# Optimization experiments

Measured on AMD Instinct MI355X. Metric: run time of the kernel, lower is better.

## Reference

```python
import jax, jax.numpy as jnp
import numpy as np

B, S, D, H = 1, 4096, 1024, 16
DH = D // H  # 64
SCALE = D ** 0.5  # original divides by input_dim**0.5, not head_dim**0.5


def setup_inputs() -> dict:
    key = jax.random.key(0)
    ks = jax.random.split(key, 11)
    s = lambda i, shape, sc=1.0: jax.random.normal(ks[i], shape, dtype=jnp.float32) * sc
    w_init = 1.0 / np.sqrt(D)
    return {
        "q": s(0, (B, S, D)),
        "k": s(1, (B, S, D)),
        "v": s(2, (B, S, D)),
        "Wq": s(3, (H, D, DH), w_init),
        "bq": jnp.zeros((H, DH), jnp.float32),
        "Wk": s(4, (H, D, DH), w_init),
        "bk": jnp.zeros((H, DH), jnp.float32),
        "Wv": s(5, (H, D, DH), w_init),
        "bv": jnp.zeros((H, DH), jnp.float32),
        "Wo": s(6, (D, D), w_init),
        "bo": jnp.zeros((D,), jnp.float32),
    }


def reference(q, k, v, Wq, bq, Wk, bk, Wv, bv, Wo, bo):
    # Per-head Dense projections, batched over heads: [B,S,D] x [H,D,dh] -> [B,H,S,dh]
    Q = jnp.einsum("bsd,hde->bhse", q, Wq) + bq[None, :, None, :]
    K = jnp.einsum("bsd,hde->bhse", k, Wk) + bk[None, :, None, :]
    V = jnp.einsum("bsd,hde->bhse", v, Wv) + bv[None, :, None, :]
    # Scaled dot-product attention; note scale = sqrt(input_dim) as in source
    scores = jnp.einsum("bhse,bhte->bhst", Q, K) / SCALE  # [B,H,S,S]
    attn = jax.nn.softmax(scores, axis=-1)
    out = jnp.einsum("bhst,bhte->bhse", attn, V)  # [B,H,S,dh]
    # Concat heads along feature dim (head order matches the Python loop)
    concat = out.transpose(0, 2, 1, 3).reshape(q.shape[0], q.shape[1], H * DH)
    return concat @ Wo + bo
```

## Files before the change

kernel.cpp:

```cpp
#include <hip/hip_runtime.h>
#include <hip/hip_bf16.h>

#define S_LEN 4096
#define D_MODEL 1024
#define NH 16
#define DHEAD 64
#define QSCALE 0.0450843293f

typedef __attribute__((ext_vector_type(8))) short short8;
typedef __attribute__((ext_vector_type(4))) float floatx4;

__device__ __forceinline__ unsigned short f2bf(float f) {
    unsigned int x = __float_as_uint(f);
    x += 0x7fffu + ((x >> 16) & 1u);
    return (unsigned short)(x >> 16);
}

__device__ __forceinline__ float exp2_fast(float x) {
    return __builtin_amdgcn_exp2f(x);
}

__device__ __forceinline__ void async_copy16(const unsigned short* g, unsigned short* l) {
    __builtin_amdgcn_global_load_lds(
        (const __attribute__((address_space(1))) void*)g,
        (__attribute__((address_space(3))) void*)l, 16, 0, 0);
}

__global__ __launch_bounds__(256) void prep_all(
    const float* __restrict__ q, const float* __restrict__ k,
    const float* __restrict__ v,
    const float* __restrict__ Wq, const float* __restrict__ Wk,
    const float* __restrict__ Wv, const float* __restrict__ Wo,
    unsigned short* __restrict__ dst, unsigned short* __restrict__ ws)
{
    __shared__ float L[64][65];
    const int tid = threadIdx.x;

    if (blockIdx.x < 6144) {
        long i = (long)(blockIdx.x * 256 + tid) * 8;
        int which = (int)(i >> 22);
        long off = i & ((1 << 22) - 1);
        const float* src = (which == 0) ? q : (which == 1) ? k : v;
        float4 f0 = *(const float4*)&src[off];
        float4 f1 = *(const float4*)&src[off + 4];
        uint4 o;
        o.x = (unsigned int)f2bf(f0.x) | ((unsigned int)f2bf(f0.y) << 16);
        o.y = (unsigned int)f2bf(f0.z) | ((unsigned int)f2bf(f0.w) << 16);
        o.z = (unsigned int)f2bf(f1.x) | ((unsigned int)f2bf(f1.y) << 16);
        o.w = (unsigned int)f2bf(f1.z) | ((unsigned int)f2bf(f1.w) << 16);
        *(uint4*)&dst[i] = o;
        return;
    }

    const int bx  = blockIdx.x - 6144;
    const int mat = bx >> 8;

    if (mat < 3) {
        const float* W = (mat == 0) ? Wq : (mat == 1) ? Wk : Wv;
        unsigned short* WT = ws + (size_t)mat * (1u << 20);
        int h  = (bx >> 4) & 15;
        int dt = bx & 15;
        #pragma unroll
        for (int i = 0; i < 16; i++) {
            int idx = i * 256 + tid;
            int dp = idx >> 6, e = idx & 63;
            L[e][dp] = W[h * 65536 + (dt * 64 + dp) * 64 + e];
        }
        __syncthreads();
        #pragma unroll
        for (int i = 0; i < 16; i++) {
            int idx = i * 256 + tid;
            int e = idx >> 6, dp = idx & 63;
            WT[(h * 64 + e) * 1024 + dt * 64 + dp] = f2bf(L[e][dp]);
        }
    } else {
        unsigned short* WoT = ws + (size_t)3 * (1u << 20);
        int rt = (bx >> 4) & 15;
        int ct = bx & 15;
        #pragma unroll
        for (int i = 0; i < 16; i++) {
            int idx = i * 256 + tid;
            int dp = idx >> 6, np = idx & 63;
            L[np][dp] = Wo[(rt * 64 + dp) * 1024 + ct * 64 + np];
        }
        __syncthreads();
        #pragma unroll
        for (int i = 0; i < 16; i++) {
            int idx = i * 256 + tid;
            int np = idx >> 6, dp = idx & 63;
            WoT[(ct * 64 + np) * 1024 + rt * 64 + dp] = f2bf(L[np][dp]);
        }
    }
}

#define GEMM_CORE(XPTR, WPTR)                                                   \
    for (int k0 = 0; k0 < D_MODEL; k0 += 64) {                                  \
        __syncthreads();                                                        \
        _Pragma("unroll")                                                       \
        for (int i = 0; i < 4; i++) {                                           \
            async_copy16(&XPTR[(size_t)(m0 + srow + i * 8) * D_MODEL + k0 + scol], \
                         &As[(wave * 32 + i * 8) * 64]);                        \
            async_copy16(&WPTR[(size_t)(n0 + srow + i * 8) * D_MODEL + k0 + scol], \
                         &Bs[(wave * 32 + i * 8) * 64]);                        \
        }                                                                       \
        __syncthreads();                                                        \
        _Pragma("unroll")                                                       \
        for (int ks = 0; ks < 2; ks++) {                                        \
            short8 af[4], bf[4];                                                \
            _Pragma("unroll")                                                   \
            for (int i = 0; i < 4; i++)                                         \
                af[i] = *(const short8*)&As[(wr * 64 + i * 16 + m) * 64 + ks * 32 + quad * 8]; \
            _Pragma("unroll")                                                   \
            for (int j = 0; j < 4; j++)                                         \
                bf[j] = *(const short8*)&Bs[(wc * 64 + j * 16 + m) * 64 + ks * 32 + quad * 8]; \
            _Pragma("unroll")                                                   \
            for (int i = 0; i < 4; i++) {                                       \
                _Pragma("unroll")                                               \
                for (int j = 0; j < 4; j++)                                     \
                    acc[i][j] = __builtin_amdgcn_mfma_f32_16x16x32_bf16(af[i], bf[j], acc[i][j], 0, 0, 0); \
            }                                                                   \
        }                                                                       \
    }

__global__ __launch_bounds__(256) void qkv_gemm(
    const unsigned short* __restrict__ Xbase, const unsigned short* __restrict__ WTbase,
    const float* __restrict__ bq, const float* __restrict__ bk,
    const float* __restrict__ bv,
    unsigned short* __restrict__ Qbuf, unsigned short* __restrict__ Kbuf,
    unsigned short* __restrict__ Vbuf)
{
    __shared__ __align__(16) unsigned short As[128 * 64];
    __shared__ __align__(16) unsigned short Bs[128 * 64];

    const int z = blockIdx.z;
    const unsigned short* X  = Xbase + (size_t)z * (4u << 20);
    const unsigned short* WT = WTbase + (size_t)z * (1u << 20);
    const float* bias = (z == 0) ? bq : (z == 1) ? bk : bv;

    const int n0 = blockIdx.x * 128;
    const int m0 = blockIdx.y * 128;
    const int tid = threadIdx.x, wave = tid >> 6, lane = tid & 63;
    const int m = lane & 15, quad = lane >> 4;
    const int wr = wave >> 1, wc = wave & 1;
    const int srow = wave * 32 + (lane >> 3);
    const int scol = (lane & 7) * 8;

    floatx4 acc[4][4];
    #pragma unroll
    for (int i = 0; i < 4; i++)
        #pragma unroll
        for (int j = 0; j < 4; j++) acc[i][j] = (floatx4){0.f, 0.f, 0.f, 0.f};

    GEMM_CORE(X, WT)

    #pragma unroll
    for (int j = 0; j < 4; j++) {
        int n = n0 + wc * 64 + j * 16 + m;
        int h = n >> 6, e = n & 63;
        float bvv = bias[n];
        #pragma unroll
        for (int i = 0; i < 4; i++) {
            int sbase = m0 + wr * 64 + i * 16 + quad * 4;
            if (z == 2) {
                ushort4 pk;
                pk.x = f2bf(acc[i][j][0] + bvv);
                pk.y = f2bf(acc[i][j][1] + bvv);
                pk.z = f2bf(acc[i][j][2] + bvv);
                pk.w = f2bf(acc[i][j][3] + bvv);
                *(ushort4*)&Vbuf[h * (DHEAD * S_LEN) + e * S_LEN + sbase] = pk;
            } else if (z == 1) {
                #pragma unroll
                for (int r = 0; r < 4; r++)
                    Kbuf[h * (S_LEN * DHEAD) + (sbase + r) * DHEAD + e] = f2bf(acc[i][j][r] + bvv);
            } else {
                #pragma unroll
                for (int r = 0; r < 4; r++)
                    Qbuf[h * (S_LEN * DHEAD) + (sbase + r) * DHEAD + e] =
                        f2bf((acc[i][j][r] + bvv) * QSCALE);
            }
        }
    }
}

__global__ __launch_bounds__(256) void out_gemm(
    const unsigned short* __restrict__ Cbuf, const unsigned short* __restrict__ WoT,
    const float* __restrict__ bo, float* __restrict__ out)
{
    __shared__ __align__(16) unsigned short As[128 * 64];
    __shared__ __align__(16) unsigned short Bs[128 * 64];

    const int n0 = blockIdx.x * 128;
    const int m0 = blockIdx.y * 128;
    const int tid = threadIdx.x, wave = tid >> 6, lane = tid & 63;
    const int m = lane & 15, quad = lane >> 4;
    const int wr = wave >> 1, wc = wave & 1;
    const int srow = wave * 32 + (lane >> 3);
    const int scol = (lane & 7) * 8;

    floatx4 acc[4][4];
    #pragma unroll
    for (int i = 0; i < 4; i++)
        #pragma unroll
        for (int j = 0; j < 4; j++) acc[i][j] = (floatx4){0.f, 0.f, 0.f, 0.f};

    GEMM_CORE(Cbuf, WoT)

    #pragma unroll
    for (int j = 0; j < 4; j++) {
        int n = n0 + wc * 64 + j * 16 + m;
        float bvv = bo[n];
        #pragma unroll
        for (int i = 0; i < 4; i++) {
            int sbase = m0 + wr * 64 + i * 16 + quad * 4;
            #pragma unroll
            for (int r = 0; r < 4; r++)
                out[(size_t)(sbase + r) * D_MODEL + n] = acc[i][j][r] + bvv;
        }
    }
}

__global__ __launch_bounds__(512) void attn_kernel(
    const unsigned short* __restrict__ Q, const unsigned short* __restrict__ K,
    const unsigned short* __restrict__ VT, unsigned short* __restrict__ concat)
{
    __shared__ __align__(16) unsigned char ldsraw[49152];
    unsigned short* lds16 = (unsigned short*)ldsraw;

    const int h  = blockIdx.y;
    const int q0 = blockIdx.x * 128;
    const unsigned short* Qh = Q  + h * (S_LEN * DHEAD);
    const unsigned short* Kh = K  + h * (S_LEN * DHEAD);
    const unsigned short* Vh = VT + h * (DHEAD * S_LEN);

    const int tid  = threadIdx.x;
    const int wave = tid >> 6;
    const int wt   = wave & 3;
    const int wq   = wave >> 2;
    const int lane = tid & 63;
    const int m    = lane & 15;
    const int quad = lane >> 4;
    const int swz  = (m & 7) << 3;
    const int lrow = lane >> 3;
    const int lcol = ((lane & 7) * 8) ^ (lrow << 3);

    unsigned short* Ps = lds16 + 16384;

    #pragma unroll
    for (int i = 0; i < 2; i++) {
        int c = 2 * wave + i;
        async_copy16(&Qh[(size_t)(q0 + 8 * c + lrow) * DHEAD + lcol], Ps + c * 512);
    }
    async_copy16(&Kh[(size_t)(8 * wave + lrow) * DHEAD + lcol], lds16 + wave * 512);
    async_copy16(&Vh[(size_t)(8 * wave + lrow) * S_LEN + lcol], lds16 + 8192 + wave * 512);
    asm volatile("s_waitcnt vmcnt(0)" ::: "memory");
    __builtin_amdgcn_s_barrier();

    short8 bq[4][2];
    #pragma unroll
    for (int qc = 0; qc < 4; qc++)
        #pragma unroll
        for (int ks = 0; ks < 2; ks++)
            bq[qc][ks] = *(const short8*)&Ps[(wq * 64 + qc * 16 + m) * 64 + ((ks * 32 + quad * 8) ^ swz)];
    __syncthreads();

    floatx4 O[4];
    #pragma unroll
    for (int nb = 0; nb < 4; nb++) O[nb] = (floatx4){0.f, 0.f, 0.f, 0.f};
    float lsum[4] = {0.f, 0.f, 0.f, 0.f};

    for (int t0 = 0; t0 < S_LEN; t0 += 64) {
        const int cur = (t0 >> 6) & 1;
        unsigned short* Ksc = lds16 + cur * 4096;
        unsigned short* Vsc = lds16 + 8192 + cur * 4096;

        if (t0) {
            asm volatile("s_waitcnt vmcnt(0)" ::: "memory");
            __builtin_amdgcn_s_barrier();
        }
        if (t0 + 64 < S_LEN) {
            unsigned short* Ksn = lds16 + (cur ^ 1) * 4096;
            unsigned short* Vsn = lds16 + 8192 + (cur ^ 1) * 4096;
            async_copy16(&Kh[(size_t)(t0 + 64 + 8 * wave + lrow) * DHEAD + lcol],
                         Ksn + wave * 512);
            async_copy16(&Vh[(size_t)(8 * wave + lrow) * S_LEN + t0 + 64 + lcol],
                         Vsn + wave * 512);
        }

        floatx4 st[4];
        #pragma unroll
        for (int qc = 0; qc < 4; qc++) st[qc] = (floatx4){0.f, 0.f, 0.f, 0.f};
        #pragma unroll
        for (int ks = 0; ks < 2; ks++) {
            short8 a = *(const short8*)&Ksc[(wt * 16 + m) * 64 + ((ks * 32 + quad * 8) ^ swz)];
            __builtin_amdgcn_s_setprio(1);
            #pragma unroll
            for (int qc = 0; qc < 4; qc++)
                st[qc] = __builtin_amdgcn_mfma_f32_16x16x32_bf16(a, bq[qc][ks], st[qc], 0, 0, 0);
            __builtin_amdgcn_s_setprio(0);
        }

        #pragma unroll
        for (int qc = 0; qc < 4; qc++) {
            float p0 = exp2_fast(st[qc][0]);
            float p1 = exp2_fast(st[qc][1]);
            float p2 = exp2_fast(st[qc][2]);
            float p3 = exp2_fast(st[qc][3]);
            lsum[qc] += (p0 + p1) + (p2 + p3);
            unsigned r0, r1;
            asm("v_cvt_pk_bf16_f32 %0, %1, %2" : "=v"(r0) : "v"(p0), "v"(p1));
            asm("v_cvt_pk_bf16_f32 %0, %1, %2" : "=v"(r1) : "v"(p2), "v"(p3));
            uint2 pk;
            pk.x = r0;
            pk.y = r1;
            *(uint2*)&Ps[(wq * 64 + qc * 16 + m) * 64 + ((wt * 16 + quad * 4) ^ swz)] = pk;
        }
        asm volatile("s_waitcnt lgkmcnt(0)" ::: "memory");
        __builtin_amdgcn_s_barrier();

        #pragma unroll
        for (int ks = 0; ks < 2; ks++) {
            short8 ap = *(const short8*)&Ps[(wave * 16 + m) * 64 + ((ks * 32 + quad * 8) ^ swz)];
            __builtin_amdgcn_s_setprio(1);
            #pragma unroll
            for (int nb = 0; nb < 4; nb++) {
                short8 bv = *(const short8*)&Vsc[(nb * 16 + m) * 64 + ((ks * 32 + quad * 8) ^ swz)];
                O[nb] = __builtin_amdgcn_mfma_f32_16x16x32_bf16(ap, bv, O[nb], 0, 0, 0);
            }
            __builtin_amdgcn_s_setprio(0);
        }
    }

    #pragma unroll
    for (int qc = 0; qc < 4; qc++) {
        lsum[qc] += __shfl_xor(lsum[qc], 16);
        lsum[qc] += __shfl_xor(lsum[qc], 32);
    }
    float* Ls = (float*)ldsraw;
    if (quad == 0) {
        #pragma unroll
        for (int qc = 0; qc < 4; qc++)
            Ls[wt * 128 + wq * 64 + qc * 16 + m] = lsum[qc];
    }
    __syncthreads();
    float linv[4];
    #pragma unroll
    for (int r = 0; r < 4; r++) {
        int qq = wave * 16 + quad * 4 + r;
        linv[r] = 1.0f / (Ls[0 * 128 + qq] + Ls[1 * 128 + qq] +
                          Ls[2 * 128 + qq] + Ls[3 * 128 + qq]);
    }

    #pragma unroll
    for (int nb = 0; nb < 4; nb++) {
        int e = nb * 16 + m;
        #pragma unroll
        for (int r = 0; r < 4; r++) {
            int s = q0 + wave * 16 + quad * 4 + r;
            concat[s * D_MODEL + h * DHEAD + e] = f2bf(O[nb][r] * linv[r]);
        }
    }
}

extern "C" void kernel_launch(void* const* d_in, const int* in_sizes, int n_in,
                              void* d_out, int out_size, void* d_ws, size_t ws_size,
                              hipStream_t stream) {
    const float* q  = (const float*)d_in[0];
    const float* k  = (const float*)d_in[1];
    const float* v  = (const float*)d_in[2];
    const float* Wq = (const float*)d_in[3];
    const float* bq = (const float*)d_in[4];
    const float* Wk = (const float*)d_in[5];
    const float* bk = (const float*)d_in[6];
    const float* Wv = (const float*)d_in[7];
    const float* bv = (const float*)d_in[8];
    const float* Wo = (const float*)d_in[9];
    const float* bo = (const float*)d_in[10];
    float* out = (float*)d_out;

    unsigned short* ws = (unsigned short*)d_ws;
    const size_t M1 = 1u << 20;
    unsigned short* WqT  = ws;
    unsigned short* WoT  = ws + 3 * M1;
    unsigned short* Qbuf = ws + 4 * M1;
    unsigned short* Kbuf = ws + 8 * M1;
    unsigned short* Vbuf = ws + 12 * M1;
    unsigned short* Cbuf = ws + 16 * M1;
    unsigned short* qb   = ws + 20 * M1;

    prep_all<<<7168, 256, 0, stream>>>(q, k, v, Wq, Wk, Wv, Wo, qb, ws);

    dim3 gq(8, 32, 3);
    qkv_gemm<<<gq, 256, 0, stream>>>(qb, WqT, bq, bk, bv, Qbuf, Kbuf, Vbuf);

    dim3 ga(32, 16);
    attn_kernel<<<ga, 512, 0, stream>>>(Qbuf, Kbuf, Vbuf, Cbuf);

    dim3 gg(8, 32);
    out_gemm<<<gg, 256, 0, stream>>>(Cbuf, WoT, bo, out);
}
```

Baseline: 272.5 us.

## Stage GEMM epilogues through LDS for coalesced stores; compute softmax sum via MFMA

The Q/K projection epilogue now writes bf16 results into a swizzled LDS tile and then stores full 16-byte rows to global memory, replacing scattered 2-byte stores. The output GEMM epilogue likewise stages fp32 results through LDS in two halves and writes float4 rows. In attention, the row sum of probabilities is computed by an extra MFMA against a ones vector, using the same bf16-rounded P values that feed the PV product. This removes per-element exp accumulation, the shuffles and the final LDS reduction. The cost is added barriers and LDS traffic in the epilogues and one extra MFMA per k-step.

```diff
diff --git a/kernel.cpp b/kernel.cpp
--- a/kernel.cpp
+++ b/kernel.cpp
@@ -129,8 +129,9 @@
     unsigned short* __restrict__ Qbuf, unsigned short* __restrict__ Kbuf,
     unsigned short* __restrict__ Vbuf)
 {
-    __shared__ __align__(16) unsigned short As[128 * 64];
-    __shared__ __align__(16) unsigned short Bs[128 * 64];
+    __shared__ __align__(16) unsigned short AB[2 * 128 * 64];
+    unsigned short* As = AB;
+    unsigned short* Bs = AB + 128 * 64;
 
     const int z = blockIdx.z;
     const unsigned short* X  = Xbase + (size_t)z * (4u << 20);
@@ -153,32 +154,56 @@
 
     GEMM_CORE(X, WT)
 
-    #pragma unroll
-    for (int j = 0; j < 4; j++) {
-        int n = n0 + wc * 64 + j * 16 + m;
-        int h = n >> 6, e = n & 63;
-        float bvv = bias[n];
-        #pragma unroll
-        for (int i = 0; i < 4; i++) {
-            int sbase = m0 + wr * 64 + i * 16 + quad * 4;
-            if (z == 2) {
+    if (z == 2) {
+        #pragma unroll
+        for (int j = 0; j < 4; j++) {
+            int n = n0 + wc * 64 + j * 16 + m;
+            int h = n >> 6, e = n & 63;
+            float bvv = bias[n];
+            #pragma unroll
+            for (int i = 0; i < 4; i++) {
+                int sbase = m0 + wr * 64 + i * 16 + quad * 4;
                 ushort4 pk;
                 pk.x = f2bf(acc[i][j][0] + bvv);
                 pk.y = f2bf(acc[i][j][1] + bvv);
                 pk.z = f2bf(acc[i][j][2] + bvv);
                 pk.w = f2bf(acc[i][j][3] + bvv);
                 *(ushort4*)&Vbuf[h * (DHEAD * S_LEN) + e * S_LEN + sbase] = pk;
-            } else if (z == 1) {
-                #pragma unroll
-                for (int r = 0; r < 4; r++)
-                    Kbuf[h * (S_LEN * DHEAD) + (sbase + r) * DHEAD + e] = f2bf(acc[i][j][r] + bvv);
-            } else {
-                #pragma unroll
-                for (int r = 0; r < 4; r++)
-                    Qbuf[h * (S_LEN * DHEAD) + (sbase + r) * DHEAD + e] =
-                        f2bf((acc[i][j][r] + bvv) * QSCALE);
             }
         }
+        return;
+    }
+
+    const float scale = (z == 0) ? QSCALE : 1.0f;
+    unsigned short* outp = (z == 0) ? Qbuf : Kbuf;
+    __syncthreads();
+    unsigned short* stage = wc ? Bs : As;
+    #pragma unroll
+    for (int j = 0; j < 4; j++) {
+        int e = j * 16 + m;
+        float bvv = bias[n0 + wc * 64 + e];
+        #pragma unroll
+        for (int i = 0; i < 4; i++) {
+            int rbase = wr * 64 + i * 16 + quad * 4;
+            #pragma unroll
+            for (int r = 0; r < 4; r++) {
+                int rowl = rbase + r;
+                stage[rowl * 64 + (e ^ ((rowl & 7) << 3))] =
+                    f2bf((acc[i][j][r] + bvv) * scale);
+            }
+        }
+    }
+    __syncthreads();
+    const int h0 = n0 >> 6;
+    const size_t base0 = (size_t)h0 * (S_LEN * DHEAD) + (size_t)m0 * DHEAD;
+    const size_t base1 = base0 + (size_t)(S_LEN * DHEAD);
+    #pragma unroll
+    for (int s = 0; s < 4; s++) {
+        int o = tid * 8 + s * 2048;
+        int row = o >> 6, c0 = o & 63;
+        int cs = c0 ^ ((row & 7) << 3);
+        *(uint4*)&outp[base0 + o] = *(const uint4*)&As[row * 64 + cs];
+        *(uint4*)&outp[base1 + o] = *(const uint4*)&Bs[row * 64 + cs];
     }
 }
 
@@ -186,8 +211,9 @@
     const unsigned short* __restrict__ Cbuf, const unsigned short* __restrict__ WoT,
     const float* __restrict__ bo, float* __restrict__ out)
 {
-    __shared__ __align__(16) unsigned short As[128 * 64];
-    __shared__ __align__(16) unsigned short Bs[128 * 64];
+    __shared__ __align__(16) unsigned short AB[2 * 128 * 64];
+    unsigned short* As = AB;
+    unsigned short* Bs = AB + 128 * 64;
 
     const int n0 = blockIdx.x * 128;
     const int m0 = blockIdx.y * 128;
@@ -205,17 +231,36 @@
 
     GEMM_CORE(Cbuf, WoT)
 
-    #pragma unroll
-    for (int j = 0; j < 4; j++) {
-        int n = n0 + wc * 64 + j * 16 + m;
-        float bvv = bo[n];
-        #pragma unroll
-        for (int i = 0; i < 4; i++) {
-            int sbase = m0 + wr * 64 + i * 16 + quad * 4;
+    __syncthreads();
+    float* Fs = (float*)AB;
+    #pragma unroll
+    for (int half = 0; half < 2; half++) {
+        if (wr == half) {
             #pragma unroll
-            for (int r = 0; r < 4; r++)
-                out[(size_t)(sbase + r) * D_MODEL + n] = acc[i][j][r] + bvv;
-        }
+            for (int j = 0; j < 4; j++) {
+                int c = wc * 64 + j * 16 + m;
+                float bvv = bo[n0 + c];
+                #pragma unroll
+                for (int i = 0; i < 4; i++) {
+                    int rbase = i * 16 + quad * 4;
+                    #pragma unroll
+                    for (int r = 0; r < 4; r++) {
+                        int rowl = rbase + r;
+                        Fs[rowl * 128 + (c ^ ((rowl & 7) << 2))] = acc[i][j][r] + bvv;
+                    }
+                }
+            }
+        }
+        __syncthreads();
+        #pragma unroll
+        for (int s = 0; s < 8; s++) {
+            int o = tid * 4 + s * 1024;
+            int row = o >> 7, c0 = o & 127;
+            int cs = c0 ^ ((row & 7) << 2);
+            *(float4*)&out[(size_t)(m0 + half * 64 + row) * D_MODEL + n0 + c0] =
+                *(const float4*)&Fs[row * 128 + cs];
+        }
+        __syncthreads();
     }
 }
 
@@ -263,10 +308,14 @@
             bq[qc][ks] = *(const short8*)&Ps[(wq * 64 + qc * 16 + m) * 64 + ((ks * 32 + quad * 8) ^ swz)];
     __syncthreads();
 
+    short8 vone;
+    #pragma unroll
+    for (int i = 0; i < 8; i++) vone[i] = (short)0x3F80;
+
     floatx4 O[4];
     #pragma unroll
     for (int nb = 0; nb < 4; nb++) O[nb] = (floatx4){0.f, 0.f, 0.f, 0.f};
-    float lsum[4] = {0.f, 0.f, 0.f, 0.f};
+    floatx4 Lacc = (floatx4){0.f, 0.f, 0.f, 0.f};
 
     for (int t0 = 0; t0 < S_LEN; t0 += 64) {
         const int cur = (t0 >> 6) & 1;
@@ -305,7 +354,6 @@
             float p1 = exp2_fast(st[qc][1]);
             float p2 = exp2_fast(st[qc][2]);
             float p3 = exp2_fast(st[qc][3]);
-            lsum[qc] += (p0 + p1) + (p2 + p3);
             unsigned r0, r1;
             asm("v_cvt_pk_bf16_f32 %0, %1, %2" : "=v"(r0) : "v"(p0), "v"(p1));
             asm("v_cvt_pk_bf16_f32 %0, %1, %2" : "=v"(r1) : "v"(p2), "v"(p3));
@@ -326,29 +374,14 @@
                 short8 bv = *(const short8*)&Vsc[(nb * 16 + m) * 64 + ((ks * 32 + quad * 8) ^ swz)];
                 O[nb] = __builtin_amdgcn_mfma_f32_16x16x32_bf16(ap, bv, O[nb], 0, 0, 0);
             }
+            Lacc = __builtin_amdgcn_mfma_f32_16x16x32_bf16(ap, vone, Lacc, 0, 0, 0);
             __builtin_amdgcn_s_setprio(0);
         }
     }
 
-    #pragma unroll
-    for (int qc = 0; qc < 4; qc++) {
-        lsum[qc] += __shfl_xor(lsum[qc], 16);
-        lsum[qc] += __shfl_xor(lsum[qc], 32);
-    }
-    float* Ls = (float*)ldsraw;
-    if (quad == 0) {
-        #pragma unroll
-        for (int qc = 0; qc < 4; qc++)
-            Ls[wt * 128 + wq * 64 + qc * 16 + m] = lsum[qc];
-    }
-    __syncthreads();
     float linv[4];
     #pragma unroll
-    for (int r = 0; r < 4; r++) {
-        int qq = wave * 16 + quad * 4 + r;
-        linv[r] = 1.0f / (Ls[0 * 128 + qq] + Ls[1 * 128 + qq] +
-                          Ls[2 * 128 + qq] + Ls[3 * 128 + qq]);
-    }
+    for (int r = 0; r < 4; r++) linv[r] = 1.0f / Lacc[r];
 
     #pragma unroll
     for (int nb = 0; nb < 4; nb++) {
```

Result: no change. 271.9 us (-0.2%).
